# Kernel tuning notes

Measured on AMD Instinct MI355X. Metric: run time of the kernel, lower is better.

## Reference

```python
import jax, jax.numpy as jnp
import numpy as np

N, D, H, C, K, NCLS, TW = 8192, 768, 4, 192, 8, 7, 1.0
HC = H * C  # 768


def setup_inputs() -> dict:
    key = jax.random.key(0)
    ks = jax.random.split(key, 40)
    gl = lambda i, shp: (jax.random.normal(ks[i], shp, jnp.float32)
                         * (1.0 / np.sqrt(shp[0] if len(shp) > 1 else shp[0])))
    inp = {"x": jax.random.normal(ks[0], (N, D), jnp.float32)}
    # BatchNorm (eval mode: running stats)
    inp["bn_gamma"] = jnp.ones((D,), jnp.float32)
    inp["bn_beta"] = jnp.zeros((D,), jnp.float32)
    inp["bn_rm"] = jnp.zeros((D,), jnp.float32)
    inp["bn_rv"] = jnp.ones((D,), jnp.float32)
    # GATConv params: W [in, H*C], att_src/att_dst [H, C], bias
    dims_in = [D, HC, HC, C]
    bias_dim = [HC, HC, C, C]  # concat,concat,mean,mean
    for li in range(4):
        b = 1 + li * 3
        inp[f"g{li+1}_w"] = gl(b, (dims_in[li], HC))
        inp[f"g{li+1}_as"] = jax.random.normal(ks[b + 1], (H, C), jnp.float32) * 0.1
        inp[f"g{li+1}_ad"] = jax.random.normal(ks[b + 2], (H, C), jnp.float32) * 0.1
        inp[f"g{li+1}_b"] = jnp.zeros((bias_dim[li],), jnp.float32)
    inp["res1_w"] = gl(14, (D, HC)); inp["res1_b"] = jnp.zeros((HC,), jnp.float32)
    inp["res2_w"] = gl(15, (HC, C)); inp["res2_b"] = jnp.zeros((C,), jnp.float32)
    for li, dim in zip(range(4), [HC, HC, C, C]):
        inp[f"ln{li+1}_g"] = jnp.ones((dim,), jnp.float32)
        inp[f"ln{li+1}_b"] = jnp.zeros((dim,), jnp.float32)
    inp["fc_w"] = gl(16, (C, NCLS)); inp["fc_b"] = jnp.zeros((NCLS,), jnp.float32)
    return inp


def _ln(x, g, b):
    mu = x.mean(-1, keepdims=True)
    v = ((x - mu) ** 2).mean(-1, keepdims=True)
    return (x - mu) * jax.lax.rsqrt(v + 1e-5) * g + b


def _build_edges(x):
    # cosine-similarity top-k graph (indices only; grads are cut upstream,
    # matching the original .item()-based host loop)
    xn = x / (jnp.linalg.norm(x, axis=1, keepdims=True) + 1e-8)
    sim = xn @ xn.T                       # [N, N]
    _, idx = jax.lax.top_k(sim, K + 1)    # first hit is self
    nbr = idx[:, 1:]                      # [N, K]
    src0 = jnp.repeat(jnp.arange(N), K)
    dst0 = nbr.reshape(-1)
    i = jnp.arange(N - 1)
    # temporal edges (i,i+1)&(i+1,i) added only if (i,i+1) not already a topk edge
    m = ~jnp.any(nbr[:-1] == (i + 1)[:, None], axis=1)
    sl = jnp.arange(N)  # self-loops (GATConv add_self_loops=True)
    src = jnp.concatenate([src0, i, i + 1, sl])
    dst = jnp.concatenate([dst0, i + 1, i, sl])
    mask = jnp.concatenate([jnp.ones(N * K, bool), m, m, jnp.ones(N, bool)])
    return src, dst, mask


def _gat(x, W, a_s, a_d, b, src, dst, mask, concat):
    n = x.shape[0]
    h = (x @ W).reshape(n, H, C)
    es = (h * a_s[None]).sum(-1)  # [N, H]
    ed = (h * a_d[None]).sum(-1)
    e = jax.nn.leaky_relu(es[src] + ed[dst], 0.2)  # [E, H]
    e = jnp.where(mask[:, None], e, -1e9)
    emax = jax.ops.segment_max(e, dst, num_segments=n)
    emax = jnp.where(jnp.isfinite(emax), emax, 0.0)
    ex = jnp.exp(e - emax[dst]) * mask[:, None].astype(e.dtype)
    denom = jax.ops.segment_sum(ex, dst, num_segments=n)
    alpha = ex / (denom[dst] + 1e-16)
    out = jax.ops.segment_sum(alpha[:, :, None] * h[src], dst, num_segments=n)
    out = out.reshape(n, HC) if concat else out.mean(1)
    return out + b


def reference(x, bn_gamma, bn_beta, bn_rm, bn_rv,
              g1_w, g1_as, g1_ad, g1_b, g2_w, g2_as, g2_ad, g2_b,
              g3_w, g3_as, g3_ad, g3_b, g4_w, g4_as, g4_ad, g4_b,
              res1_w, res1_b, res2_w, res2_b,
              ln1_g, ln1_b, ln2_g, ln2_b, ln3_g, ln3_b, ln4_g, ln4_b,
              fc_w, fc_b):
    xb = (x - bn_rm) * jax.lax.rsqrt(bn_rv + 1e-5) * bn_gamma + bn_beta
    src, dst, mask = _build_edges(jax.lax.stop_gradient(xb))
    r = xb @ res1_w + res1_b
    h = _gat(xb, g1_w, g1_as, g1_ad, g1_b, src, dst, mask, True)
    h = _ln(jax.nn.relu(h) + r, ln1_g, ln1_b)
    r = h
    h = _gat(h, g2_w, g2_as, g2_ad, g2_b, src, dst, mask, True)
    h = _ln(jax.nn.relu(h) + r, ln2_g, ln2_b)
    r = h @ res2_w + res2_b
    h = _gat(h, g3_w, g3_as, g3_ad, g3_b, src, dst, mask, False)
    h = _ln(jax.nn.relu(h) + r, ln3_g, ln3_b)
    r = h
    h = _gat(h, g4_w, g4_as, g4_ad, g4_b, src, dst, mask, False)
    h = _ln(jax.nn.relu(h) + r, ln4_g, ln4_b)
    return h @ fc_w + fc_b
```

## Files before the change

### kernel.cpp

```cpp
#include <hip/hip_runtime.h>
#include <hip/hip_bf16.h>

#define NN 8192
#define DD 768
#define HH 4
#define CC 192
#define KK 8
#define HC 768

typedef __attribute__((ext_vector_type(8))) short short8;
typedef __attribute__((ext_vector_type(4))) float floatx4;

static __device__ __forceinline__ short f2bf(float v) {
    unsigned u = __builtin_bit_cast(unsigned, v);
    u += 0x7fff + ((u >> 16) & 1);
    return (short)(u >> 16);
}
static __device__ __forceinline__ float bf2f(short s) {
    unsigned u = ((unsigned)(unsigned short)s) << 16;
    return __builtin_bit_cast(float, u);
}

static __device__ __forceinline__ void gl16(const void* g, void* l) {
    __builtin_amdgcn_global_load_lds(
        (__attribute__((address_space(1))) void*)(void*)g,
        (__attribute__((address_space(3))) void*)l, 16, 0, 0);
}

__global__ __launch_bounds__(256) void bnorm_kernel(const float* __restrict__ x,
    const float* __restrict__ g, const float* __restrict__ b,
    const float* __restrict__ rm, const float* __restrict__ rv,
    short* __restrict__ xbh, short* __restrict__ xbl,
    short* __restrict__ xnh, short* __restrict__ xnl)
{
    int i = blockIdx.x, t = threadIdx.x;
    __shared__ float red[256];
    float v[3];
    float ss = 0.f;
#pragma unroll
    for (int q = 0; q < 3; q++) {
        int d = t + q * 256;
        float xv = x[(size_t)i * DD + d];
        float vv = (xv - rm[d]) * rsqrtf(rv[d] + 1e-5f) * g[d] + b[d];
        v[q] = vv; ss += vv * vv;
    }
    red[t] = ss; __syncthreads();
    for (int s = 128; s; s >>= 1) { if (t < s) red[t] += red[t + s]; __syncthreads(); }
    float inv = 1.0f / (sqrtf(red[0]) + 1e-8f);
#pragma unroll
    for (int q = 0; q < 3; q++) {
        int d = t + q * 256;
        size_t idx = (size_t)i * DD + d;
        float vv = v[q];
        short h = f2bf(vv);
        xbh[idx] = h; xbl[idx] = f2bf(vv - bf2f(h));
        float nv = vv * inv;
        short nh = f2bf(nv);
        xnh[idx] = nh; xnl[idx] = f2bf(nv - bf2f(nh));
    }
}

__global__ __launch_bounds__(256) void wtrans6(
    const float* w0, short* o0h, short* o0l,
    const float* w1, short* o1h, short* o1l,
    const float* w2, short* o2h, short* o2l,
    const float* w3, short* o3h, short* o3l,
    const float* w4, short* o4h, short* o4l,
    const float* w5, short* o5h, short* o5l)
{
    int idx = blockIdx.x * 256 + threadIdx.x;
    const float* w; short* oh; short* ol; int K, P; int r;
    if (idx < 589824)            { w = w0; oh = o0h; ol = o0l; K = 768; P = 768; r = idx; }
    else if (idx < 2 * 589824)   { w = w1; oh = o1h; ol = o1l; K = 768; P = 768; r = idx - 589824; }
    else if (idx < 3 * 589824)   { w = w2; oh = o2h; ol = o2l; K = 768; P = 768; r = idx - 2 * 589824; }
    else if (idx < 3 * 589824 + 147456) { w = w3; oh = o3h; ol = o3l; K = 768; P = 192; r = idx - 3 * 589824; }
    else if (idx < 4 * 589824 + 147456) { w = w4; oh = o4h; ol = o4l; K = 768; P = 768; r = idx - 3 * 589824 - 147456; }
    else if (idx < 4 * 589824 + 2 * 147456) { w = w5; oh = o5h; ol = o5l; K = 192; P = 768; r = idx - 4 * 589824 - 147456; }
    else return;
    int p = r / K, k = r % K;
    float v = w[(size_t)k * P + p];
    short h = f2bf(v);
    oh[r] = h;
    ol[r] = f2bf(v - bf2f(h));
}

__global__ __launch_bounds__(256) void mfma_nt(
    const short* __restrict__ Ahi, const short* __restrict__ Alo,
    const short* __restrict__ Bhi, const short* __restrict__ Blo,
    const float* __restrict__ bias, int biasN,
    float* __restrict__ C, int Cstride,
    short* __restrict__ Cbf, int bfoff, int bfstride,
    const float* __restrict__ a_s, const float* __restrict__ a_d,
    float* __restrict__ es, float* __restrict__ ed, int hoff,
    int M, int K, int P)
{
    __shared__ __attribute__((aligned(16))) short sAh[128 * 32];
    __shared__ __attribute__((aligned(16))) short sAl[128 * 32];
    __shared__ __attribute__((aligned(16))) short sBh[128 * 32];
    __shared__ __attribute__((aligned(16))) short sBl[128 * 32];
    int t = threadIdx.x;
    int wave = t >> 6, lane = t & 63;
    int wm = wave & 1, wn = wave >> 1;
    int i0 = blockIdx.y * 128, j0 = blockIdx.x * 128;
    int mrow = lane & 15, quad = lane >> 4;

    int srow = lane >> 2;
    int kg   = (lane & 3) ^ ((lane >> 3) & 3);
    int koff = kg * 8;
    int c0 = wave * 2, c1 = c0 + 1;
    int ar0 = i0 + c0 * 16 + srow, ar1 = i0 + c1 * 16 + srow;
    int br0 = j0 + c0 * 16 + srow, br1 = j0 + c1 * 16 + srow;
    if (br0 > P - 1) br0 = P - 1;
    if (br1 > P - 1) br1 = P - 1;
    const short* pAh0 = Ahi + (size_t)ar0 * K + koff;
    const short* pAh1 = Ahi + (size_t)ar1 * K + koff;
    const short* pAl0 = Alo + (size_t)ar0 * K + koff;
    const short* pAl1 = Alo + (size_t)ar1 * K + koff;
    const short* pBh0 = Bhi + (size_t)br0 * K + koff;
    const short* pBh1 = Bhi + (size_t)br1 * K + koff;
    const short* pBl0 = Blo + (size_t)br0 * K + koff;
    const short* pBl1 = Blo + (size_t)br1 * K + koff;
    short* dA0 = sAh + c0 * 512; short* dA1 = sAh + c1 * 512;
    short* dAl0 = sAl + c0 * 512; short* dAl1 = sAl + c1 * 512;
    short* dB0 = sBh + c0 * 512; short* dB1 = sBh + c1 * 512;
    short* dBl0 = sBl + c0 * 512; short* dBl1 = sBl + c1 * 512;

    floatx4 acc[4][4];
#pragma unroll
    for (int a = 0; a < 4; a++)
#pragma unroll
        for (int b = 0; b < 4; b++) acc[a][b] = (floatx4){0.f, 0.f, 0.f, 0.f};

    int aoff[4], boff[4];
#pragma unroll
    for (int mt = 0; mt < 4; mt++) {
        int r = wm * 64 + mt * 16 + mrow;
        aoff[mt] = r * 32 + (quad ^ ((r >> 1) & 3)) * 8;
    }
#pragma unroll
    for (int nt = 0; nt < 4; nt++) {
        int r = wn * 64 + nt * 16 + mrow;
        boff[nt] = r * 32 + (quad ^ ((r >> 1) & 3)) * 8;
    }

    for (int k0 = 0; k0 < K; k0 += 32) {
        gl16(pAh0 + k0, dA0);  gl16(pAh1 + k0, dA1);
        gl16(pAl0 + k0, dAl0); gl16(pAl1 + k0, dAl1);
        gl16(pBh0 + k0, dB0);  gl16(pBh1 + k0, dB1);
        gl16(pBl0 + k0, dBl0); gl16(pBl1 + k0, dBl1);
        __syncthreads();

        short8 ah[4], al[4], bh[4], bl[4];
#pragma unroll
        for (int mt = 0; mt < 4; mt++) {
            ah[mt] = *(const short8*)(sAh + aoff[mt]);
            al[mt] = *(const short8*)(sAl + aoff[mt]);
        }
#pragma unroll
        for (int nt = 0; nt < 4; nt++) {
            bh[nt] = *(const short8*)(sBh + boff[nt]);
            bl[nt] = *(const short8*)(sBl + boff[nt]);
        }
#pragma unroll
        for (int mt = 0; mt < 4; mt++)
#pragma unroll
            for (int nt = 0; nt < 4; nt++) {
                acc[mt][nt] = __builtin_amdgcn_mfma_f32_16x16x32_bf16(
                    ah[mt], bh[nt], acc[mt][nt], 0, 0, 0);
                acc[mt][nt] = __builtin_amdgcn_mfma_f32_16x16x32_bf16(
                    ah[mt], bl[nt], acc[mt][nt], 0, 0, 0);
                acc[mt][nt] = __builtin_amdgcn_mfma_f32_16x16x32_bf16(
                    al[mt], bh[nt], acc[mt][nt], 0, 0, 0);
            }
        __syncthreads();
    }

#pragma unroll
    for (int mt = 0; mt < 4; mt++)
#pragma unroll
        for (int nt = 0; nt < 4; nt++) {
            int col = j0 + wn * 64 + nt * 16 + mrow;
            if (col < P) {
                if (col < bfoff) {
                    float bb = (bias && col < biasN) ? bias[col] : 0.f;
#pragma unroll
                    for (int r = 0; r < 4; r++) {
                        int row = i0 + wm * 64 + mt * 16 + quad * 4 + r;
                        C[(size_t)row * Cstride + col] = acc[mt][nt][r] + bb;
                    }
                } else {
#pragma unroll
                    for (int r = 0; r < 4; r++) {
                        int row = i0 + wm * 64 + mt * 16 + quad * 4 + r;
                        Cbf[(size_t)row * bfstride + col - bfoff] = f2bf(acc[mt][nt][r]);
                    }
                }
            }
        }

    if (a_s) {
        int base = j0 + wn * 64;
        if (base >= hoff && base + 64 <= P) {
            int head = (base - hoff) / CC;
            int cb = (base - hoff) % CC;
#pragma unroll
            for (int mt = 0; mt < 4; mt++) {
                float ps[4] = {0.f, 0.f, 0.f, 0.f};
                float pd[4] = {0.f, 0.f, 0.f, 0.f};
#pragma unroll
                for (int nt = 0; nt < 4; nt++) {
                    int c = cb + nt * 16 + mrow;
                    float as_ = a_s[head * CC + c];
                    float ad_ = a_d[head * CC + c];
#pragma unroll
                    for (int r = 0; r < 4; r++) {
                        ps[r] += acc[mt][nt][r] * as_;
                        pd[r] += acc[mt][nt][r] * ad_;
                    }
                }
#pragma unroll
                for (int off = 1; off < 16; off <<= 1)
#pragma unroll
                    for (int r = 0; r < 4; r++) {
                        ps[r] += __shfl_xor(ps[r], off);
                        pd[r] += __shfl_xor(pd[r], off);
                    }
                if (mrow == 0) {
#pragma unroll
                    for (int r = 0; r < 4; r++) {
                        int row = i0 + wm * 64 + mt * 16 + quad * 4 + r;
                        atomicAdd(&es[row * 4 + head], ps[r]);
                        atomicAdd(&ed[row * 4 + head], pd[r]);
                    }
                }
            }
        }
    }
}

__device__ __forceinline__ bool tk_try(float* v, int* id, float xv, int xi)
{
    if (xv > v[8] || (xv == v[8] && xi < id[8])) {
        v[8] = xv; id[8] = xi;
#pragma unroll
        for (int p = 8; p > 0; p--) {
            if (v[p] > v[p - 1] || (v[p] == v[p - 1] && id[p] < id[p - 1])) {
                float tv = v[p]; v[p] = v[p - 1]; v[p - 1] = tv;
                int ti2 = id[p]; id[p] = id[p - 1]; id[p - 1] = ti2;
            } else break;
        }
        return true;
    }
    return false;
}

__global__ __launch_bounds__(256) void topk1_kernel(const float* __restrict__ sim,
    float* __restrict__ pv, int* __restrict__ pi)
{
    int wave = threadIdx.x >> 6, lane = threadIdx.x & 63;
    int task = blockIdx.x * 4 + wave;
    int row = task >> 3, seg = task & 7;
    const float4* p4 = (const float4*)(sim + (size_t)row * NN + seg * 1024);

    float4 f0 = p4[lane], f1 = p4[lane + 64], f2 = p4[lane + 128], f3 = p4[lane + 192];
    float v[9]; int id[9];
#pragma unroll
    for (int q = 0; q < 9; q++) { v[q] = -3e38f; id[q] = 0x7fffffff; }
    int jb = seg * 1024 + lane * 4;
#pragma unroll
    for (int g = 0; g < 4; g++) {
        float4 f = g == 0 ? f0 : (g == 1 ? f1 : (g == 2 ? f2 : f3));
        float gm = fmaxf(fmaxf(f.x, f.y), fmaxf(f.z, f.w));
        if (gm >= v[8]) {
            int j = jb + g * 256;
            tk_try(v, id, f.x, j);
            tk_try(v, id, f.y, j + 1);
            tk_try(v, id, f.z, j + 2);
            tk_try(v, id, f.w, j + 3);
        }
    }
    float wv = -3e38f; int wi = 0x7fffffff;
#pragma unroll
    for (int r = 0; r < 9; r++) {
        float bv = v[0]; int bi = id[0];
#pragma unroll
        for (int off = 1; off < 64; off <<= 1) {
            float ov = __shfl_xor(bv, off);
            int oi = __shfl_xor(bi, off);
            if (ov > bv || (ov == bv && oi < bi)) { bv = ov; bi = oi; }
        }
        if (id[0] == bi) {
#pragma unroll
            for (int q = 0; q < 8; q++) { v[q] = v[q + 1]; id[q] = id[q + 1]; }
            v[8] = -3e38f; id[8] = 0x7fffffff;
        }
        if (lane == r) { wv = bv; wi = bi; }
    }
    if (lane < 9) {
        size_t o = (size_t)task * 9 + lane;
        pv[o] = wv; pi[o] = wi;
    }
}

__global__ __launch_bounds__(256) void topk2_kernel(const float* __restrict__ pv,
    const int* __restrict__ pi, int* __restrict__ nbr, int r0)
{
    int wave = threadIdx.x >> 6, lane = threadIdx.x & 63;
    int row = blockIdx.x * 4 + wave;
    size_t base = (size_t)row * 72;
    float v[2]; int id[2];
    v[0] = -3e38f; id[0] = 0x7fffffff;
    v[1] = -3e38f; id[1] = 0x7fffffff;
    if (lane < 72) { v[0] = pv[base + lane]; id[0] = pi[base + lane]; }
    if (lane < 8)  { v[1] = pv[base + 64 + lane]; id[1] = pi[base + 64 + lane]; }
    if (v[1] > v[0] || (v[1] == v[0] && id[1] < id[0])) {
        float tv = v[0]; v[0] = v[1]; v[1] = tv;
        int ti = id[0]; id[0] = id[1]; id[1] = ti;
    }
    int myi = 0;
#pragma unroll
    for (int r = 0; r < 9; r++) {
        float bv = v[0]; int bi = id[0];
#pragma unroll
        for (int off = 1; off < 64; off <<= 1) {
            float ov = __shfl_xor(bv, off);
            int oi = __shfl_xor(bi, off);
            if (ov > bv || (ov == bv && oi < bi)) { bv = ov; bi = oi; }
        }
        if (id[0] == bi) {
            v[0] = v[1]; id[0] = id[1];
            v[1] = -3e38f; id[1] = 0x7fffffff;
        }
        if (r >= 1 && lane == r - 1) myi = bi;
    }
    if (lane < KK) nbr[(size_t)(r0 + row) * KK + lane] = myi;
}

__global__ __launch_bounds__(256) void count_kernel(const int* __restrict__ nbr,
                                                    int* __restrict__ deg, int* __restrict__ mfl)
{
    int i = blockIdx.x * 256 + threadIdx.x;
    if (i >= NN) return;
    atomicAdd(&deg[i], 1);
    int mm = 0;
#pragma unroll
    for (int k = 0; k < KK; k++) {
        int j = nbr[i * KK + k];
        atomicAdd(&deg[j], 1);
        if (j == i + 1) mm = 1;
    }
    if (i < NN - 1) {
        mfl[i] = !mm;
        if (!mm) { atomicAdd(&deg[i + 1], 1); atomicAdd(&deg[i], 1); }
    }
}

__global__ __launch_bounds__(256) void scan_kernel(const int* __restrict__ deg,
                                                   int* __restrict__ rowptr, int* __restrict__ cur)
{
    __shared__ int sums[256];
    int t = threadIdx.x;
    int loc[32];
    int base = t * 32;
    int s = 0;
#pragma unroll
    for (int q = 0; q < 32; q++) { loc[q] = s; s += deg[base + q]; }
    sums[t] = s; __syncthreads();
    for (int off = 1; off < 256; off <<= 1) {
        int v = (t >= off) ? sums[t - off] : 0;
        __syncthreads();
        sums[t] += v;
        __syncthreads();
    }
    int myoff = (t == 0) ? 0 : sums[t - 1];
#pragma unroll
    for (int q = 0; q < 32; q++) { int rp = myoff + loc[q]; rowptr[base + q] = rp; cur[base + q] = rp; }
    if (t == 255) rowptr[NN] = sums[255];
}

__global__ __launch_bounds__(256) void fill_kernel(const int* __restrict__ nbr,
    const int* __restrict__ mfl, int* __restrict__ cur, int* __restrict__ csr)
{
    int i = blockIdx.x * 256 + threadIdx.x;
    if (i >= NN) return;
    int pos = atomicAdd(&cur[i], 1); csr[pos] = i;
#pragma unroll
    for (int k = 0; k < KK; k++) {
        int j = nbr[i * KK + k];
        pos = atomicAdd(&cur[j], 1); csr[pos] = i;
    }
    if (i < NN - 1 && mfl[i]) {
        pos = atomicAdd(&cur[i + 1], 1); csr[pos] = i;
        pos = atomicAdd(&cur[i], 1); csr[pos] = i + 1;
    }
}

__global__ __launch_bounds__(256) void agg_ln_kernel(const short* __restrict__ h, int hst,
    const float* __restrict__ es, const float* __restrict__ ed,
    const int* __restrict__ rowptr, const int* __restrict__ csr,
    const float* __restrict__ gb, const float* __restrict__ rres, int rst,
    const float* __restrict__ gamma, const float* __restrict__ beta,
    float* __restrict__ outp, short* __restrict__ ohi, short* __restrict__ olo,
    int Dm, int concat,
    const float* __restrict__ fcw, const float* __restrict__ fcb,
    float* __restrict__ fco)
{
    int j = blockIdx.x;
    int t = threadIdx.x;
    int lane = t & 63, wave = t >> 6;
    __shared__ int ssrc[256];
    __shared__ float sal[256 * 4];
    __shared__ float sred[1024];
    __shared__ float accs[768];
    int p0 = rowptr[j], p1 = rowptr[j + 1];
    int cnt = p1 - p0;
    float edj[4];
#pragma unroll
    for (int hd = 0; hd < 4; hd++) edj[hd] = ed[j * 4 + hd];

    float acc0 = 0.f, acc1 = 0.f, acc2 = 0.f;
    int d0 = t, d1 = t + 256, d2 = t + 512;
    int h0 = d0 / CC, h1_ = d1 / CC, h2_ = d2 / CC;

    if (cnt <= 256) {
        float e[4];
        if (t < cnt) {
            int s = csr[p0 + t];
            ssrc[t] = s;
#pragma unroll
            for (int hd = 0; hd < 4; hd++) {
                float ee = es[s * 4 + hd] + edj[hd];
                e[hd] = ee > 0.f ? ee : 0.2f * ee;
            }
        } else {
#pragma unroll
            for (int hd = 0; hd < 4; hd++) e[hd] = -1e30f;
        }
        float mh[4];
#pragma unroll
        for (int hd = 0; hd < 4; hd++) {
            float rv = e[hd];
#pragma unroll
            for (int off = 32; off; off >>= 1) rv = fmaxf(rv, __shfl_down(rv, off));
            if (lane == 0) sred[wave * 4 + hd] = rv;
        }
        __syncthreads();
#pragma unroll
        for (int hd = 0; hd < 4; hd++)
            mh[hd] = fmaxf(fmaxf(sred[hd], sred[4 + hd]), fmaxf(sred[8 + hd], sred[12 + hd]));
        __syncthreads();
        float ex[4];
#pragma unroll
        for (int hd = 0; hd < 4; hd++) {
            ex[hd] = (t < cnt) ? expf(e[hd] - mh[hd]) : 0.f;
            float rv = ex[hd];
#pragma unroll
            for (int off = 32; off; off >>= 1) rv += __shfl_down(rv, off);
            if (lane == 0) sred[wave * 4 + hd] = rv;
        }
        __syncthreads();
#pragma unroll
        for (int hd = 0; hd < 4; hd++) {
            float dh = sred[hd] + sred[4 + hd] + sred[8 + hd] + sred[12 + hd] + 1e-16f;
            if (t < cnt) sal[t * 4 + hd] = ex[hd] / dh;
        }
        __syncthreads();
        for (int e2 = 0; e2 < cnt; e2++) {
            const short* hs = h + (size_t)ssrc[e2] * hst;
            acc0 += sal[e2 * 4 + h0] * bf2f(hs[d0]);
            acc1 += sal[e2 * 4 + h1_] * bf2f(hs[d1]);
            acc2 += sal[e2 * 4 + h2_] * bf2f(hs[d2]);
        }
    } else {
        float mh[4] = {-1e30f, -1e30f, -1e30f, -1e30f};
        for (int p = p0 + t; p < p1; p += 256) {
            int s = csr[p];
#pragma unroll
            for (int hd = 0; hd < 4; hd++) {
                float e = es[s * 4 + hd] + edj[hd];
                e = e > 0.f ? e : 0.2f * e;
                mh[hd] = fmaxf(mh[hd], e);
            }
        }
#pragma unroll
        for (int hd = 0; hd < 4; hd++) sred[hd * 256 + t] = mh[hd];
        __syncthreads();
        for (int s2 = 128; s2; s2 >>= 1) {
            if (t < s2)
#pragma unroll
                for (int hd = 0; hd < 4; hd++)
                    sred[hd * 256 + t] = fmaxf(sred[hd * 256 + t], sred[hd * 256 + t + s2]);
            __syncthreads();
        }
#pragma unroll
        for (int hd = 0; hd < 4; hd++) mh[hd] = sred[hd * 256];
        __syncthreads();
        float sh[4] = {0.f, 0.f, 0.f, 0.f};
        for (int p = p0 + t; p < p1; p += 256) {
            int s = csr[p];
#pragma unroll
            for (int hd = 0; hd < 4; hd++) {
                float e = es[s * 4 + hd] + edj[hd];
                e = e > 0.f ? e : 0.2f * e;
                sh[hd] += expf(e - mh[hd]);
            }
        }
#pragma unroll
        for (int hd = 0; hd < 4; hd++) sred[hd * 256 + t] = sh[hd];
        __syncthreads();
        for (int s2 = 128; s2; s2 >>= 1) {
            if (t < s2)
#pragma unroll
                for (int hd = 0; hd < 4; hd++)
                    sred[hd * 256 + t] += sred[hd * 256 + t + s2];
            __syncthreads();
        }
        float dh[4];
#pragma unroll
        for (int hd = 0; hd < 4; hd++) dh[hd] = sred[hd * 256] + 1e-16f;
        __syncthreads();
        for (int p = p0; p < p1; p += 64) {
            int cn = min(64, p1 - p);
            if (t < cn) {
                int s = csr[p + t];
                ssrc[t] = s;
#pragma unroll
                for (int hd = 0; hd < 4; hd++) {
                    float e = es[s * 4 + hd] + edj[hd];
                    e = e > 0.f ? e : 0.2f * e;
                    sal[t * 4 + hd] = expf(e - mh[hd]) / dh[hd];
                }
            }
            __syncthreads();
            for (int e2 = 0; e2 < cn; e2++) {
                const short* hs = h + (size_t)ssrc[e2] * hst;
                acc0 += sal[e2 * 4 + h0] * bf2f(hs[d0]);
                acc1 += sal[e2 * 4 + h1_] * bf2f(hs[d1]);
                acc2 += sal[e2 * 4 + h2_] * bf2f(hs[d2]);
            }
            __syncthreads();
        }
    }

    if (concat) {
        float v0 = fmaxf(acc0 + gb[d0], 0.f) + rres[(size_t)j * rst + d0];
        float v1 = fmaxf(acc1 + gb[d1], 0.f) + rres[(size_t)j * rst + d1];
        float v2 = fmaxf(acc2 + gb[d2], 0.f) + rres[(size_t)j * rst + d2];
        __syncthreads();
        sred[t] = v0 + v1 + v2; __syncthreads();
        for (int s = 128; s; s >>= 1) { if (t < s) sred[t] += sred[t + s]; __syncthreads(); }
        float mu = sred[0] / 768.f;
        __syncthreads();
        float a0 = v0 - mu, a1 = v1 - mu, a2 = v2 - mu;
        sred[t] = a0 * a0 + a1 * a1 + a2 * a2; __syncthreads();
        for (int s = 128; s; s >>= 1) { if (t < s) sred[t] += sred[t + s]; __syncthreads(); }
        float rs = rsqrtf(sred[0] / 768.f + 1e-5f);
        size_t base = (size_t)j * 768;
        float w0 = a0 * rs * gamma[d0] + beta[d0];
        float w1 = a1 * rs * gamma[d1] + beta[d1];
        float w2 = a2 * rs * gamma[d2] + beta[d2];
        if (outp) { outp[base + d0] = w0; outp[base + d1] = w1; outp[base + d2] = w2; }
        short hh;
        hh = f2bf(w0); ohi[base + d0] = hh; olo[base + d0] = f2bf(w0 - bf2f(hh));
        hh = f2bf(w1); ohi[base + d1] = hh; olo[base + d1] = f2bf(w1 - bf2f(hh));
        hh = f2bf(w2); ohi[base + d2] = hh; olo[base + d2] = f2bf(w2 - bf2f(hh));
    } else {
        accs[d0] = acc0; accs[d1] = acc1; accs[d2] = acc2;
        __syncthreads();
        float val = 0.f;
        if (t < CC)
            val = fmaxf((accs[t] + accs[t + CC] + accs[t + 2 * CC] + accs[t + 3 * CC]) * 0.25f
                        + gb[t], 0.f) + rres[(size_t)j * rst + t];
        __syncthreads();
        sred[t] = (t < CC) ? val : 0.f; __syncthreads();
        for (int s = 128; s; s >>= 1) { if (t < s) sred[t] += sred[t + s]; __syncthreads(); }
        float mu = sred[0] / (float)CC;
        __syncthreads();
        float a = val - mu;
        sred[t] = (t < CC) ? a * a : 0.f; __syncthreads();
        for (int s = 128; s; s >>= 1) { if (t < s) sred[t] += sred[t + s]; __syncthreads(); }
        float rs = rsqrtf(sred[0] / (float)CC + 1e-5f);
        float w = a * rs * ((t < CC) ? gamma[t] : 0.f) + ((t < CC) ? beta[t] : 0.f);
        if (t < CC) {
            size_t idx = (size_t)j * CC + t;
            if (outp) outp[idx] = w;
            if (ohi) {
                short hh = f2bf(w);
                ohi[idx] = hh; olo[idx] = f2bf(w - bf2f(hh));
            }
            accs[t] = w;
        }
        if (fco) {
            __syncthreads();
            if (t < 64) {
#pragma unroll
                for (int n = 0; n < 7; n++) {
                    float p = 0.f;
                    for (int d = t; d < CC; d += 64) p += accs[d] * fcw[d * 7 + n];
#pragma unroll
                    for (int off = 32; off; off >>= 1) p += __shfl_down(p, off);
                    if (t == 0) fco[(size_t)j * 7 + n] = p + fcb[n];
                }
            }
        }
    }
}

extern "C" void kernel_launch(void* const* d_in, const int* in_sizes, int n_in,
                              void* d_out, int out_size, void* d_ws, size_t ws_size,
                              hipStream_t stream)
{
    const float* x     = (const float*)d_in[0];
    const float* bn_g  = (const float*)d_in[1];
    const float* bn_b  = (const float*)d_in[2];
    const float* bn_rm = (const float*)d_in[3];
    const float* bn_rv = (const float*)d_in[4];
    const float* g_w[4]  = {(const float*)d_in[5], (const float*)d_in[9],
                            (const float*)d_in[13], (const float*)d_in[17]};
    const float* g_as[4] = {(const float*)d_in[6], (const float*)d_in[10],
                            (const float*)d_in[14], (const float*)d_in[18]};
    const float* g_ad[4] = {(const float*)d_in[7], (const float*)d_in[11],
                            (const float*)d_in[15], (const float*)d_in[19]};
    const float* g_b[4]  = {(const float*)d_in[8], (const float*)d_in[12],
                            (const float*)d_in[16], (const float*)d_in[20]};
    const float* res1_w = (const float*)d_in[21];
    const float* res1_b = (const float*)d_in[22];
    const float* res2_w = (const float*)d_in[23];
    const float* res2_b = (const float*)d_in[24];
    const float* ln_g[4] = {(const float*)d_in[25], (const float*)d_in[27],
                            (const float*)d_in[29], (const float*)d_in[31]};
    const float* ln_b[4] = {(const float*)d_in[26], (const float*)d_in[28],
                            (const float*)d_in[30], (const float*)d_in[32]};
    const float* fc_w = (const float*)d_in[33];
    const float* fc_b = (const float*)d_in[34];
    float* out = (float*)d_out;

    float* F = (float*)d_ws;
    float* ASIM = F; F += 16777216;
    float* R1   = F; F += 6291456;
    float* H1   = F; F += 6291456;
    float* R2   = F; F += 1572864;
    float* H3   = F; F += 1572864;
    float* ESB  = F; F += 262144;
    short* S = (short*)F;
    short* XNH = S; S += 6291456;
    short* XNL = S; S += 6291456;
    short* XAH = S; S += 6291456;
    short* XAL = S; S += 6291456;
    short* HBH = S; S += 6291456;
    short* WT1H = S; S += 1179648;
    short* WT1L = S; S += 1179648;
    short* WT2H = S; S += 589824;
    short* WT2L = S; S += 589824;
    short* WT3H = S; S += 737280;
    short* WT3L = S; S += 737280;
    short* WT4H = S; S += 147456;
    short* WT4L = S; S += 147456;
    int* I = (int*)S;
    int* NBR    = I; I += NN * KK;
    int* DEG    = I; I += NN;
    int* ROWPTR = I; I += NN + 8;
    int* CUR    = I; I += NN;
    int* MFL    = I; I += NN;
    int* CSR    = I; I += 131072;
    float* PV   = (float*)I; I += 147456;
    int* PI     = I; I += 147456;
    float* ES[4], *ED[4];
    for (int l = 0; l < 4; l++) { ES[l] = ESB + l * 65536; ED[l] = ES[l] + 32768; }

    bnorm_kernel<<<NN, 256, 0, stream>>>(x, bn_g, bn_b, bn_rm, bn_rv,
                                         XAH, XAL, XNH, XNL);
    hipMemsetAsync(ESB, 0, 262144 * sizeof(float), stream);
    hipMemsetAsync(DEG, 0, NN * sizeof(int), stream);
    wtrans6<<<(4 * 589824 + 2 * 147456 + 255) / 256, 256, 0, stream>>>(
        res1_w, WT1H, WT1L,
        g_w[0], WT1H + 768 * 768, WT1L + 768 * 768,
        g_w[1], WT2H, WT2L,
        res2_w, WT3H, WT3L,
        g_w[2], WT3H + 192 * 768, WT3L + 192 * 768,
        g_w[3], WT4H, WT4L);
    for (int ch = 0; ch < 4; ch++) {
        mfma_nt<<<dim3(NN / 128, 2048 / 128), 256, 0, stream>>>(
            XNH + (size_t)ch * 2048 * DD, XNL + (size_t)ch * 2048 * DD,
            XNH, XNL, nullptr, 0, ASIM, NN, nullptr, 0x7fffffff, 0,
            nullptr, nullptr, nullptr, nullptr, 0, 2048, DD, NN);
        topk1_kernel<<<4096, 256, 0, stream>>>(ASIM, PV, PI);
        topk2_kernel<<<512, 256, 0, stream>>>(PV, PI, NBR, ch * 2048);
    }
    count_kernel<<<NN / 256, 256, 0, stream>>>(NBR, DEG, MFL);
    scan_kernel<<<1, 256, 0, stream>>>(DEG, ROWPTR, CUR);
    fill_kernel<<<NN / 256, 256, 0, stream>>>(NBR, MFL, CUR, CSR);
    mfma_nt<<<dim3(12, NN / 128), 256, 0, stream>>>(XAH, XAL, WT1H, WT1L,
        res1_b, 768, R1, 768, HBH, 768, 768,
        g_as[0], g_ad[0], ES[0], ED[0], 768, NN, DD, 1536);
    agg_ln_kernel<<<NN, 256, 0, stream>>>(HBH, 768, ES[0], ED[0], ROWPTR, CSR,
        g_b[0], R1, 768, ln_g[0], ln_b[0], H1, XAH, XAL, HC, 1, nullptr, nullptr, nullptr);
    mfma_nt<<<dim3(6, NN / 128), 256, 0, stream>>>(XAH, XAL, WT2H, WT2L,
        nullptr, 0, nullptr, 0, HBH, 0, 768,
        g_as[1], g_ad[1], ES[1], ED[1], 0, NN, HC, HC);
    agg_ln_kernel<<<NN, 256, 0, stream>>>(HBH, 768, ES[1], ED[1], ROWPTR, CSR,
        g_b[1], H1, 768, ln_g[1], ln_b[1], nullptr, XAH, XAL, HC, 1, nullptr, nullptr, nullptr);
    mfma_nt<<<dim3(8, NN / 128), 256, 0, stream>>>(XAH, XAL, WT3H, WT3L,
        res2_b, 192, R2, 192, HBH, 192, 768,
        g_as[2], g_ad[2], ES[2], ED[2], 192, NN, HC, 960);
    agg_ln_kernel<<<NN, 256, 0, stream>>>(HBH, 768, ES[2], ED[2], ROWPTR, CSR,
        g_b[2], R2, 192, ln_g[2], ln_b[2], H3, XAH, XAL, CC, 0, nullptr, nullptr, nullptr);
    mfma_nt<<<dim3(6, NN / 128), 256, 0, stream>>>(XAH, XAL, WT4H, WT4L,
        nullptr, 0, nullptr, 0, HBH, 0, 768,
        g_as[3], g_ad[3], ES[3], ED[3], 0, NN, CC, HC);
    agg_ln_kernel<<<NN, 256, 0, stream>>>(HBH, 768, ES[3], ED[3], ROWPTR, CSR,
        g_b[3], H3, 192, ln_g[3], ln_b[3], nullptr, nullptr, nullptr, CC, 0, fc_w, fc_b, out);
}
```

Before: 1.208 ms.

## Exploit symmetry of cosine similarity matrix to halve GEMM work

Computes the similarity matrix in 4096-row blocks: the off-diagonal block once with a transposed mirror store through LDS, and diagonal blocks over upper-triangle tiles only, mirroring the rest. Top-k partials are written per 1024-column segment into a larger buffer and merged once. This removes redundant MFMA work in the symmetric product at the cost of extra transposed stores and workspace aliasing.

```diff
diff --git a/kernel.cpp b/kernel.cpp
--- a/kernel.cpp
+++ b/kernel.cpp
@@ -82,6 +82,137 @@
     short h = f2bf(v);
     oh[r] = h;
     ol[r] = f2bf(v - bf2f(h));
+}
+
+__global__ __launch_bounds__(256) void mfma_sym(
+    const short* __restrict__ Xh, const short* __restrict__ Xl,
+    int rowa, int rowb, int diag,
+    float* __restrict__ Cab, float* __restrict__ Cba)
+{
+    __shared__ __attribute__((aligned(16))) float fsm[64 * 129];
+    short* sAh = (short*)fsm;
+    short* sAl = (short*)fsm + 4096;
+    short* sBh = (short*)fsm + 8192;
+    short* sBl = (short*)fsm + 12288;
+    int t = threadIdx.x;
+    int wave = t >> 6, lane = t & 63;
+    int wm = wave & 1, wn = wave >> 1;
+    int bi, bj;
+    if (diag) {
+        int L = blockIdx.x;
+        int j = (int)((sqrtf(8.f * (float)L + 1.f) - 1.f) * 0.5f);
+        while (j * (j + 1) / 2 > L) j--;
+        while ((j + 1) * (j + 2) / 2 <= L) j++;
+        bi = L - j * (j + 1) / 2; bj = j;
+    } else { bi = blockIdx.y; bj = blockIdx.x; }
+    int i0 = bi * 128, j0 = bj * 128;
+    int mrow = lane & 15, quad = lane >> 4;
+
+    int srow = lane >> 2;
+    int kg   = (lane & 3) ^ ((lane >> 3) & 3);
+    int koff = kg * 8;
+    int c0 = wave * 2, c1 = c0 + 1;
+    int ar0 = rowa + i0 + c0 * 16 + srow, ar1 = rowa + i0 + c1 * 16 + srow;
+    int br0 = rowb + j0 + c0 * 16 + srow, br1 = rowb + j0 + c1 * 16 + srow;
+    const short* pAh0 = Xh + (size_t)ar0 * DD + koff;
+    const short* pAh1 = Xh + (size_t)ar1 * DD + koff;
+    const short* pAl0 = Xl + (size_t)ar0 * DD + koff;
+    const short* pAl1 = Xl + (size_t)ar1 * DD + koff;
+    const short* pBh0 = Xh + (size_t)br0 * DD + koff;
+    const short* pBh1 = Xh + (size_t)br1 * DD + koff;
+    const short* pBl0 = Xl + (size_t)br0 * DD + koff;
+    const short* pBl1 = Xl + (size_t)br1 * DD + koff;
+    short* dA0 = sAh + c0 * 512; short* dA1 = sAh + c1 * 512;
+    short* dAl0 = sAl + c0 * 512; short* dAl1 = sAl + c1 * 512;
+    short* dB0 = sBh + c0 * 512; short* dB1 = sBh + c1 * 512;
+    short* dBl0 = sBl + c0 * 512; short* dBl1 = sBl + c1 * 512;
+
+    floatx4 acc[4][4];
+#pragma unroll
+    for (int a = 0; a < 4; a++)
+#pragma unroll
+        for (int b = 0; b < 4; b++) acc[a][b] = (floatx4){0.f, 0.f, 0.f, 0.f};
+
+    int aoff[4], boff[4];
+#pragma unroll
+    for (int mt = 0; mt < 4; mt++) {
+        int r = wm * 64 + mt * 16 + mrow;
+        aoff[mt] = r * 32 + (quad ^ ((r >> 1) & 3)) * 8;
+    }
+#pragma unroll
+    for (int nt = 0; nt < 4; nt++) {
+        int r = wn * 64 + nt * 16 + mrow;
+        boff[nt] = r * 32 + (quad ^ ((r >> 1) & 3)) * 8;
+    }
+
+    for (int k0 = 0; k0 < DD; k0 += 32) {
+        gl16(pAh0 + k0, dA0);  gl16(pAh1 + k0, dA1);
+        gl16(pAl0 + k0, dAl0); gl16(pAl1 + k0, dAl1);
+        gl16(pBh0 + k0, dB0);  gl16(pBh1 + k0, dB1);
+        gl16(pBl0 + k0, dBl0); gl16(pBl1 + k0, dBl1);
+        __syncthreads();
+
+        short8 ah[4], al[4], bh[4], bl[4];
+#pragma unroll
+        for (int mt = 0; mt < 4; mt++) {
+            ah[mt] = *(const short8*)(sAh + aoff[mt]);
+            al[mt] = *(const short8*)(sAl + aoff[mt]);
+        }
+#pragma unroll
+        for (int nt = 0; nt < 4; nt++) {
+            bh[nt] = *(const short8*)(sBh + boff[nt]);
+            bl[nt] = *(const short8*)(sBl + boff[nt]);
+        }
+#pragma unroll
+        for (int mt = 0; mt < 4; mt++)
+#pragma unroll
+            for (int nt = 0; nt < 4; nt++) {
+                acc[mt][nt] = __builtin_amdgcn_mfma_f32_16x16x32_bf16(
+                    ah[mt], bh[nt], acc[mt][nt], 0, 0, 0);
+                acc[mt][nt] = __builtin_amdgcn_mfma_f32_16x16x32_bf16(
+                    ah[mt], bl[nt], acc[mt][nt], 0, 0, 0);
+                acc[mt][nt] = __builtin_amdgcn_mfma_f32_16x16x32_bf16(
+                    al[mt], bh[nt], acc[mt][nt], 0, 0, 0);
+            }
+        __syncthreads();
+    }
+
+#pragma unroll
+    for (int mt = 0; mt < 4; mt++)
+#pragma unroll
+        for (int nt = 0; nt < 4; nt++) {
+            int col = j0 + wn * 64 + nt * 16 + mrow;
+#pragma unroll
+            for (int r = 0; r < 4; r++) {
+                int row = i0 + wm * 64 + mt * 16 + quad * 4 + r;
+                Cab[(size_t)row * 4096 + col] = acc[mt][nt][r];
+            }
+        }
+
+    if (!diag || bi != bj) {
+        float* Cm = Cba;
+        for (int half = 0; half < 2; half++) {
+            __syncthreads();
+            if (wn == half) {
+#pragma unroll
+                for (int mt = 0; mt < 4; mt++)
+#pragma unroll
+                    for (int nt = 0; nt < 4; nt++)
+#pragma unroll
+                        for (int r = 0; r < 4; r++) {
+                            int c = nt * 16 + mrow;
+                            int rr = wm * 64 + mt * 16 + quad * 4 + r;
+                            fsm[c * 129 + rr] = acc[mt][nt][r];
+                        }
+            }
+            __syncthreads();
+            for (int it = 0; it < 32; it++) {
+                int idx = it * 256 + t;
+                int lr = idx >> 7, lc = idx & 127;
+                Cm[(size_t)(j0 + half * 64 + lr) * 4096 + i0 + lc] = fsm[lr * 129 + lc];
+            }
+        }
+    }
 }
 
 __global__ __launch_bounds__(256) void mfma_nt(
@@ -254,19 +385,20 @@
     return false;
 }
 
-__global__ __launch_bounds__(256) void topk1_kernel(const float* __restrict__ sim,
-    float* __restrict__ pv, int* __restrict__ pi)
+__global__ __launch_bounds__(256) void topk1p_kernel(const float* __restrict__ sim,
+    float* __restrict__ pv, int* __restrict__ pi,
+    int rowbase, int segbase, int colbase)
 {
     int wave = threadIdx.x >> 6, lane = threadIdx.x & 63;
     int task = blockIdx.x * 4 + wave;
-    int row = task >> 3, seg = task & 7;
-    const float4* p4 = (const float4*)(sim + (size_t)row * NN + seg * 1024);
+    int row = task >> 2, seg = task & 3;
+    const float4* p4 = (const float4*)(sim + (size_t)row * 4096 + seg * 1024);
 
     float4 f0 = p4[lane], f1 = p4[lane + 64], f2 = p4[lane + 128], f3 = p4[lane + 192];
     float v[9]; int id[9];
 #pragma unroll
     for (int q = 0; q < 9; q++) { v[q] = -3e38f; id[q] = 0x7fffffff; }
-    int jb = seg * 1024 + lane * 4;
+    int jb = colbase + seg * 1024 + lane * 4;
 #pragma unroll
     for (int g = 0; g < 4; g++) {
         float4 f = g == 0 ? f0 : (g == 1 ? f1 : (g == 2 ? f2 : f3));
@@ -297,7 +429,7 @@
         if (lane == r) { wv = bv; wi = bi; }
     }
     if (lane < 9) {
-        size_t o = (size_t)task * 9 + lane;
+        size_t o = ((size_t)(rowbase + row) * 8 + segbase + seg) * 9 + lane;
         pv[o] = wv; pi[o] = wi;
     }
 }
@@ -636,12 +768,14 @@
     float* out = (float*)d_out;
 
     float* F = (float*)d_ws;
-    float* ASIM = F; F += 16777216;
-    float* R1   = F; F += 6291456;
-    float* H1   = F; F += 6291456;
-    float* R2   = F; F += 1572864;
-    float* H3   = F; F += 1572864;
-    float* ESB  = F; F += 262144;
+    float* SAB  = F; F += 16777216;
+    float* UNI  = F; F += 16777216;
+    float* SBA = UNI;
+    float* R1  = UNI;
+    float* H1  = R1 + 6291456;
+    float* R2  = H1 + 6291456;
+    float* H3  = R2 + 1572864;
+    float* ESB = H3 + 1572864;
     short* S = (short*)F;
     short* XNH = S; S += 6291456;
     short* XNL = S; S += 6291456;
@@ -663,14 +797,13 @@
     int* CUR    = I; I += NN;
     int* MFL    = I; I += NN;
     int* CSR    = I; I += 131072;
-    float* PV   = (float*)I; I += 147456;
-    int* PI     = I; I += 147456;
+    float* PV   = (float*)I; I += 589824;
+    int* PI     = I; I += 589824;
     float* ES[4], *ED[4];
     for (int l = 0; l < 4; l++) { ES[l] = ESB + l * 65536; ED[l] = ES[l] + 32768; }
 
     bnorm_kernel<<<NN, 256, 0, stream>>>(x, bn_g, bn_b, bn_rm, bn_rv,
                                          XAH, XAL, XNH, XNL);
-    hipMemsetAsync(ESB, 0, 262144 * sizeof(float), stream);
     hipMemsetAsync(DEG, 0, NN * sizeof(int), stream);
     wtrans6<<<(4 * 589824 + 2 * 147456 + 255) / 256, 256, 0, stream>>>(
         res1_w, WT1H, WT1L,
@@ -679,17 +812,18 @@
         res2_w, WT3H, WT3L,
         g_w[2], WT3H + 192 * 768, WT3L + 192 * 768,
         g_w[3], WT4H, WT4L);
-    for (int ch = 0; ch < 4; ch++) {
-        mfma_nt<<<dim3(NN / 128, 2048 / 128), 256, 0, stream>>>(
-            XNH + (size_t)ch * 2048 * DD, XNL + (size_t)ch * 2048 * DD,
-            XNH, XNL, nullptr, 0, ASIM, NN, nullptr, 0x7fffffff, 0,
-            nullptr, nullptr, nullptr, nullptr, 0, 2048, DD, NN);
-        topk1_kernel<<<4096, 256, 0, stream>>>(ASIM, PV, PI);
-        topk2_kernel<<<512, 256, 0, stream>>>(PV, PI, NBR, ch * 2048);
-    }
+    mfma_sym<<<dim3(32, 32), 256, 0, stream>>>(XNH, XNL, 0, 4096, 0, SAB, SBA);
+    topk1p_kernel<<<4096, 256, 0, stream>>>(SAB, PV, PI, 0, 4, 4096);
+    topk1p_kernel<<<4096, 256, 0, stream>>>(SBA, PV, PI, 4096, 0, 0);
+    mfma_sym<<<528, 256, 0, stream>>>(XNH, XNL, 0, 0, 1, SAB, SAB);
+    topk1p_kernel<<<4096, 256, 0, stream>>>(SAB, PV, PI, 0, 0, 0);
+    mfma_sym<<<528, 256, 0, stream>>>(XNH, XNL, 4096, 4096, 1, SBA, SBA);
+    topk1p_kernel<<<4096, 256, 0, stream>>>(SBA, PV, PI, 4096, 4, 4096);
+    topk2_kernel<<<NN / 4, 256, 0, stream>>>(PV, PI, NBR, 0);
     count_kernel<<<NN / 256, 256, 0, stream>>>(NBR, DEG, MFL);
     scan_kernel<<<1, 256, 0, stream>>>(DEG, ROWPTR, CUR);
     fill_kernel<<<NN / 256, 256, 0, stream>>>(NBR, MFL, CUR, CSR);
+    hipMemsetAsync(ESB, 0, 262144 * sizeof(float), stream);
     mfma_nt<<<dim3(12, NN / 128), 256, 0, stream>>>(XAH, XAL, WT1H, WT1L,
         res1_b, 768, R1, 768, HBH, 768, 768,
         g_as[0], g_ad[0], ES[0], ED[0], 768, NN, DD, 1536);
```

Result: faster. 1.085 ms (-10.2%).
